# Optimization experiments

Measured on AMD Instinct MI355X. Metric: run time of the kernel, lower is better.

The kernel has to match this reference:

```python
import jax, jax.numpy as jnp
import numpy as np

INF = 1e10
EPS = 1e-5
B, S, H, NH = 4, 1024, 1024, 16


def _linear(x, W, b):
    return x @ W + b


def _layernorm(x, g, b):
    mean = x.mean(-1, keepdims=True)
    var = ((x - mean) ** 2).mean(-1, keepdims=True)  # biased, matches .pow(2).mean
    return g * (x - mean) / jnp.sqrt(var + EPS) + b


def _mha(xq, xkv, mask, Wq, bq, Wk, bk, Wv, bv, Wo, bo, num_head):
    Bq, Sq, Hd = xq.shape
    d = Hd // num_head
    scale = jnp.asarray(np.sqrt(d), xq.dtype)
    q = _linear(xq, Wq, bq).reshape(Bq, Sq, num_head, d).transpose(0, 2, 1, 3)
    k = _linear(xkv, Wk, bk).reshape(Bq, -1, num_head, d).transpose(0, 2, 1, 3)
    v = _linear(xkv, Wv, bv).reshape(Bq, -1, num_head, d).transpose(0, 2, 1, 3)
    scores = jnp.einsum('bhqd,bhkd->bhqk', q, k) / scale
    # mask [B,Skv] -> additive; NOTE: original divides (scores+mask) by scale AGAIN
    add = (1.0 - mask[:, None, None, :].astype(scores.dtype)) * (-INF)
    att = jax.nn.softmax((scores + add) / scale, axis=-1)
    out = jnp.einsum('bhqk,bhkd->bhqd', att, v).transpose(0, 2, 1, 3).reshape(Bq, Sq, Hd)
    return _linear(out, Wo, bo)


def _block(hidden_states, self_att_mask, cross_hidden_states, cross_att_mask,
           sWq, sbq, sWk, sbk, sWv, sbv, sWo, sbo,
           cWq, cbq, cWk, cbk, cWv, cbv, cWo, cbo,
           g, b, W1, b1, W2, b2, num_head):
    sa = _mha(hidden_states, hidden_states, self_att_mask,
              sWq, sbq, sWk, sbk, sWv, sbv, sWo, sbo, num_head)
    sa_n = _layernorm(sa + hidden_states, g, b)
    ca = _mha(sa_n, cross_hidden_states, cross_att_mask,
              cWq, cbq, cWk, cbk, cWv, cbv, cWo, cbo, num_head)
    # NOTE: residual uses the ORIGINAL hidden_states, matching the source
    h = _layernorm(ca + hidden_states, g, b)
    ff = _linear(jax.nn.relu(_linear(h, W1, b1)), W2, b2)
    return _layernorm(ff + h, g, b)


def setup_inputs() -> dict:
    key = jax.random.key(0)
    ks = jax.random.split(key, 20)
    std = 0.02
    def lin(k, din, dout):
        k1, k2 = jax.random.split(k)
        return (jax.random.normal(k1, (din, dout), jnp.float32) * std,
                jax.random.normal(k2, (dout,), jnp.float32) * std)
    inp = {
        'hidden_states': jax.random.normal(ks[0], (B, S, H), jnp.float32),
        'self_att_mask': jnp.ones((B, S), jnp.int32),
        'cross_hidden_states': jax.random.normal(ks[1], (B, S, H), jnp.float32),
        'cross_att_mask': jnp.ones((B, S), jnp.int32),
        'num_head': NH,
    }
    names = ['sWq sbq', 'sWk sbk', 'sWv sbv', 'sWo sbo',
             'cWq cbq', 'cWk cbk', 'cWv cbv', 'cWo cbo']
    for i, nm in enumerate(names):
        wn, bn = nm.split()
        W, bb = lin(ks[2 + i], H, H)
        inp[wn] = W
        inp[bn] = bb
    inp['g'] = jnp.ones((H,), jnp.float32)
    inp['b'] = jnp.zeros((H,), jnp.float32)
    inp['W1'], inp['b1'] = lin(ks[12], H, 4 * H)
    inp['W2'], inp['b2'] = lin(ks[13], 4 * H, H)
    return inp


def reference(hidden_states, self_att_mask, cross_hidden_states, cross_att_mask,
              num_head, sWq, sbq, sWk, sbk, sWv, sbv, sWo, sbo,
              cWq, cbq, cWk, cbk, cWv, cbv, cWo, cbo,
              g, b, W1, b1, W2, b2):
    return _block(hidden_states, self_att_mask, cross_hidden_states, cross_att_mask,
                  sWq, sbq, sWk, sbk, sWv, sbv, sWo, sbo,
                  cWq, cbq, cWk, cbk, cWv, cbv, cWo, cbo,
                  g, b, W1, b1, W2, b2, num_head)
```

## Files before the change

### kernel.cpp

```cpp
#include <hip/hip_runtime.h>
#include <hip/hip_bf16.h>


typedef float float4v __attribute__((ext_vector_type(4)));
typedef __bf16 bf16x8 __attribute__((ext_vector_type(8)));
typedef unsigned short ushort8 __attribute__((ext_vector_type(8)));
typedef unsigned int uint2v __attribute__((ext_vector_type(2)));

#define VBIG (1 << 29)

__device__ __forceinline__ unsigned short f2bf1(float f) {
    unsigned u = __builtin_bit_cast(unsigned, f);
    u += 0x7fffu + ((u >> 16) & 1u);
    return (unsigned short)(u >> 16);
}
__device__ __forceinline__ unsigned f2bf2(float lo, float hi) {
    unsigned a = __builtin_bit_cast(unsigned, lo);
    a += 0x7fffu + ((a >> 16) & 1u);
    unsigned b = __builtin_bit_cast(unsigned, hi);
    b += 0x7fffu + ((b >> 16) & 1u);
    return (a >> 16) | (b & 0xffff0000u);
}
__device__ __forceinline__ float4v bf4_to_f4(uint2v u) {
    float4v r;
    r.x = __builtin_bit_cast(float, (u.x & 0xffffu) << 16);
    r.y = __builtin_bit_cast(float, u.x & 0xffff0000u);
    r.z = __builtin_bit_cast(float, (u.y & 0xffffu) << 16);
    r.w = __builtin_bit_cast(float, u.y & 0xffff0000u);
    return r;
}
__device__ __forceinline__ bf16x8 ldsv8(const unsigned short* p) {
    return __builtin_bit_cast(bf16x8, *(const ushort8*)p);
}
__device__ __forceinline__ void async16(const unsigned short* g, unsigned short* l) {
    __builtin_amdgcn_global_load_lds(
        (const __attribute__((address_space(1))) unsigned int*)(g),
        (__attribute__((address_space(3))) unsigned int*)(l),
        16, 0, 0);
}

template <int RELU, int DBUF>
__device__ __forceinline__ void gemm_core(
    const unsigned short* __restrict__ A, const unsigned short* __restrict__ Bt,
    const float* __restrict__ bias, unsigned short* __restrict__ Cout,
    int m0, int n0, int K, int KL, int kbase, int ldc,
    float qs, int vrel, unsigned short* __restrict__ VTout, size_t outoff)
{
    __shared__ __align__(16) unsigned short As[(DBUF ? 2 : 1) * 128 * 64];
    __shared__ __align__(16) unsigned short Bs[(DBUF ? 2 : 1) * 128 * 64];

    const int tid = threadIdx.x;
    const int w = tid >> 6, lane = tid & 63;
    const int lr = lane & 15, quad = lane >> 4;
    const int wm = (w >> 1) * 64, wn = (w & 1) * 64;

    const int sr = lane >> 3, sc = lane & 7;
    const int fch = sc ^ sr;
    const unsigned short* Ag = A + (size_t)(m0 + w * 32 + sr) * K + kbase + fch * 8;
    const unsigned short* Bg = Bt + (size_t)(n0 + w * 32 + sr) * K + kbase + fch * 8;

    float4v acc[4][4];
#pragma unroll
    for (int i = 0; i < 4; i++)
#pragma unroll
        for (int j = 0; j < 4; j++) acc[i][j] = 0.f;

    const int ch0 = quad ^ (lr & 7);
    const int ch1 = (4 + quad) ^ (lr & 7);

    auto issue = [&](int buf, int k0) {
        unsigned short* Al = &As[buf * (128 * 64) + (w * 32) * 64];
        unsigned short* Bl = &Bs[buf * (128 * 64) + (w * 32) * 64];
#pragma unroll
        for (int i = 0; i < 4; i++) {
            async16(Ag + (size_t)(i * 8) * K + k0, Al + (i * 8) * 64);
            async16(Bg + (size_t)(i * 8) * K + k0, Bl + (i * 8) * 64);
        }
    };
    auto compute = [&](int buf) {
        const unsigned short* Ab = &As[buf * (128 * 64)];
        const unsigned short* Bb = &Bs[buf * (128 * 64)];
#pragma unroll
        for (int kk = 0; kk < 2; kk++) {
            const int ch = kk ? ch1 : ch0;
            bf16x8 af[4], bf[4];
#pragma unroll
            for (int i = 0; i < 4; i++) {
                af[i] = ldsv8(&Ab[(wm + i * 16 + lr) * 64 + ch * 8]);
                bf[i] = ldsv8(&Bb[(wn + i * 16 + lr) * 64 + ch * 8]);
            }
#pragma unroll
            for (int i = 0; i < 4; i++)
#pragma unroll
                for (int j = 0; j < 4; j++)
                    acc[i][j] = __builtin_amdgcn_mfma_f32_16x16x32_bf16(af[i], bf[j], acc[i][j], 0, 0, 0);
        }
    };

    if (DBUF) {
        const int NIT = KL >> 6;
        issue(0, 0);
        for (int it = 0; it < NIT; ++it) {
            const int nxt = it + 1;
            if (nxt < NIT) {
                issue(nxt & 1, nxt << 6);
                __builtin_amdgcn_sched_barrier(0);
                __builtin_amdgcn_s_waitcnt(0x0F78);
            } else {
                __builtin_amdgcn_sched_barrier(0);
                __builtin_amdgcn_s_waitcnt(0x0F70);
            }
            __builtin_amdgcn_s_barrier();
            __builtin_amdgcn_sched_barrier(0);
            compute(it & 1);
            __builtin_amdgcn_sched_barrier(0);
            __builtin_amdgcn_s_barrier();
            __builtin_amdgcn_sched_barrier(0);
        }
    } else {
        for (int k0 = 0; k0 < KL; k0 += 64) {
            issue(0, k0);
            __syncthreads();
            compute(0);
            __syncthreads();
        }
    }

    if (vrel >= 0) {
        const int crel = vrel + wn;
        const int hh = crel >> 6;
        const int bidx = (m0 + wm) >> 10;
        const int tbase = ((m0 + wm) & 1023) + quad * 16;
#pragma unroll
        for (int j = 0; j < 4; j++) {
            const float bv = bias ? bias[n0 + wn + j * 16 + lr] : 0.f;
            const int d = j * 16 + lr;
            unsigned short* vp = VTout + ((size_t)(bidx * 16 + hh) * 64 + d) * 1024 + tbase;
#pragma unroll
            for (int r = 0; r < 4; r++) {
                uint2v u = { f2bf2(acc[0][j][r] + bv, acc[1][j][r] + bv),
                             f2bf2(acc[2][j][r] + bv, acc[3][j][r] + bv) };
                *(uint2v*)(vp + r * 4) = u;
            }
        }
        return;
    }

#pragma unroll
    for (int j = 0; j < 4; j++) {
        const int col = n0 + wn + j * 16 + lr;
        const float bv = bias ? bias[col] : 0.f;
#pragma unroll
        for (int i = 0; i < 4; i++) {
            const int row0 = m0 + wm + i * 16 + quad * 4;
#pragma unroll
            for (int r = 0; r < 4; r++) {
                float v = (acc[i][j][r] + bv) * qs;
                if (RELU) v = fmaxf(v, 0.f);
                Cout[outoff + (size_t)(row0 + r) * ldc + col] = f2bf1(v);
            }
        }
    }
}

template <int RELU, int DBUF>
__global__ __launch_bounds__(256) void gemm_bt(
    const unsigned short* __restrict__ A, const unsigned short* __restrict__ Bt,
    const float* __restrict__ bias, unsigned short* __restrict__ Cout,
    int M, int N, int K, int ldc, int order, int qcols, int vcol0,
    unsigned short* __restrict__ VTout)
{
    const int m0 = (order ? blockIdx.x : blockIdx.y) * 128;
    const int n0 = (order ? blockIdx.y : blockIdx.x) * 128;
    const int KL = K / gridDim.z;
    const int kbase = blockIdx.z * KL;
    const float qs = (n0 < qcols) ? 0.015625f : 1.0f;
    const int vrel = (n0 >= vcol0) ? n0 - vcol0 : -1;
    const size_t outoff = (size_t)blockIdx.z * M * ldc;
    gemm_core<RELU, DBUF>(A, Bt, bias, Cout, m0, n0, K, KL, kbase, ldc,
                          qs, vrel, VTout, outoff);
}

__global__ __launch_bounds__(256) void gemm_cross(
    const unsigned short* __restrict__ SANb, const unsigned short* __restrict__ WtCWQ,
    const float* __restrict__ cbq, unsigned short* __restrict__ CQ,
    const unsigned short* __restrict__ cxb, const unsigned short* __restrict__ WtCKV,
    const float* __restrict__ biasC, unsigned short* __restrict__ CKb,
    unsigned short* __restrict__ VTc)
{
    const int m0 = blockIdx.x * 128;
    const int y = blockIdx.y;
    const unsigned short *Ax, *Btx;
    const float* bx;
    unsigned short* Cx = nullptr;
    unsigned short* vt = nullptr;
    int n0, ldc = 1024, vrel = -1;
    float qs = 1.0f;
    if (y < 8) {
        Ax = SANb; Btx = WtCWQ; bx = cbq; Cx = CQ; n0 = y * 128; qs = 0.015625f;
    } else {
        Ax = cxb; Btx = WtCKV; bx = biasC; n0 = (y - 8) * 128;
        if (n0 < 1024) Cx = CKb;
        else { vrel = n0 - 1024; vt = VTc; }
    }
    gemm_core<0, 0>(Ax, Btx, bx, Cx, m0, n0, 1024, 1024, 0, ldc, qs, vrel, vt, 0);
}

__global__ __launch_bounds__(256) void attn_mfma(
    const unsigned short* __restrict__ Q, int qs,
    const unsigned short* __restrict__ K, int kvs,
    const unsigned short* __restrict__ VT,
    const float* __restrict__ maskf,
    unsigned short* __restrict__ O)
{
    __shared__ __align__(16) unsigned short Ks[2][64 * 64];
    __shared__ __align__(16) unsigned short Vt[2][64 * 64];
    __shared__ __align__(16) unsigned short Pb[64 * 64];
    __shared__ float msk[1024];

    const int bid = blockIdx.x;
    const int jdx = (bid & 7) * 128 + (bid >> 3);
    const int q0 = (jdx & 15) * 64, h = (jdx >> 4) & 15, b = jdx >> 8;
    const int tid = threadIdx.x;
    const int w = tid >> 6, lane = tid & 63;
    const int lr = lane & 15, quad = lane >> 4;
    const int wm = w * 16;
    const float4v zf = {0.f, 0.f, 0.f, 0.f};

    ((float4v*)msk)[tid] = ((const float4v*)(maskf + b * 1024))[tid];

    bf16x8 qf[2];
#pragma unroll
    for (int c = 0; c < 2; c++)
        qf[c] = ldsv8(Q + (size_t)(b * 1024 + q0 + wm + lr) * qs
                      + h * 64 + c * 32 + quad * 8);

    const int sr = lane >> 3, sc = lane & 7;
    const int fch = sc ^ sr;
    const int ch0 = quad ^ (lr & 7), ch1 = (4 + quad) ^ (lr & 7);
    const unsigned short* VTb = VT + (size_t)(b * 16 + h) * 64 * 1024;

    __syncthreads();

    float4v oac[4];
    float lsum[4];
#pragma unroll
    for (int jj = 0; jj < 4; jj++) { oac[jj] = zf; lsum[jj] = 0.f; }

    auto issue = [&](int kb, int buf) {
        const int s0 = kb * 64;
#pragma unroll
        for (int i = 0; i < 2; i++) {
            async16(K + (size_t)(b * 1024 + s0 + w * 16 + i * 8 + sr) * kvs + h * 64 + fch * 8,
                    &Ks[buf][(w * 16 + i * 8) * 64]);
            async16(VTb + (size_t)(w * 16 + i * 8 + sr) * 1024 + s0 + fch * 8,
                    &Vt[buf][(w * 16 + i * 8) * 64]);
        }
    };

    issue(0, 0);
    for (int kb = 0; kb < 16; ++kb) {
        const int cur = kb & 1;
        const int nxt = kb + 1;
        if (nxt < 16) {
            issue(nxt, nxt & 1);
            __builtin_amdgcn_sched_barrier(0);
            __builtin_amdgcn_s_waitcnt(0x0F74);
        } else {
            __builtin_amdgcn_sched_barrier(0);
            __builtin_amdgcn_s_waitcnt(0x0F70);
        }
        __builtin_amdgcn_s_barrier();
        __builtin_amdgcn_sched_barrier(0);

        float mf[4];
#pragma unroll
        for (int jj = 0; jj < 4; jj++)
            mf[jj] = msk[kb * 64 + jj * 16 + lr];

        float4v sa[4];
        __builtin_amdgcn_s_setprio(1);
#pragma unroll
        for (int jj = 0; jj < 4; jj++) {
            const int krow = jj * 16 + lr;
            bf16x8 kf0 = ldsv8(&Ks[cur][krow * 64 + ch0 * 8]);
            bf16x8 kf1 = ldsv8(&Ks[cur][krow * 64 + ch1 * 8]);
            sa[jj] = __builtin_amdgcn_mfma_f32_16x16x32_bf16(qf[0], kf0, zf, 0, 0, 0);
            sa[jj] = __builtin_amdgcn_mfma_f32_16x16x32_bf16(qf[1], kf1, sa[jj], 0, 0, 0);
        }
        __builtin_amdgcn_s_setprio(0);

#pragma unroll
        for (int rr = 0; rr < 4; rr++) {
            const float p0 = __expf(sa[0][rr]) * mf[0];
            const float p1 = __expf(sa[1][rr]) * mf[1];
            const float p2 = __expf(sa[2][rr]) * mf[2];
            const float p3 = __expf(sa[3][rr]) * mf[3];
            lsum[rr] += (p0 + p1) + (p2 + p3);
            const int row = wm + quad * 4 + rr;
            const int schp = (lr >> 1) ^ (row & 7);
            uint2v pk = { f2bf2(p0, p1), f2bf2(p2, p3) };
            *(uint2v*)&Pb[row * 64 + schp * 8 + (lr & 1) * 4] = pk;
        }

        bf16x8 pf[2];
#pragma unroll
        for (int c = 0; c < 2; c++)
            pf[c] = ldsv8(&Pb[(wm + lr) * 64 + (c ? ch1 : ch0) * 8]);
        __builtin_amdgcn_s_setprio(1);
#pragma unroll
        for (int jj = 0; jj < 4; jj++) {
            bf16x8 vf0 = ldsv8(&Vt[cur][(jj * 16 + lr) * 64 + ch0 * 8]);
            bf16x8 vf1 = ldsv8(&Vt[cur][(jj * 16 + lr) * 64 + ch1 * 8]);
            oac[jj] = __builtin_amdgcn_mfma_f32_16x16x32_bf16(pf[0], vf0, oac[jj], 0, 0, 0);
            oac[jj] = __builtin_amdgcn_mfma_f32_16x16x32_bf16(pf[1], vf1, oac[jj], 0, 0, 0);
        }
        __builtin_amdgcn_s_setprio(0);

        __builtin_amdgcn_sched_barrier(0);
        __builtin_amdgcn_s_barrier();
        __builtin_amdgcn_sched_barrier(0);
    }

#pragma unroll
    for (int rr = 0; rr < 4; rr++) {
        float l = lsum[rr];
        l += __shfl_xor(l, 1);
        l += __shfl_xor(l, 2);
        l += __shfl_xor(l, 4);
        l += __shfl_xor(l, 8);
        const float inv = 1.0f / l;
        const int row = q0 + wm + quad * 4 + rr;
        unsigned short* op = O + (size_t)(b * 1024 + row) * 1024 + h * 64;
#pragma unroll
        for (int jj = 0; jj < 4; jj++)
            op[jj * 16 + lr] = f2bf1(oac[jj][rr] * inv);
    }
}

#define PSTRIDE ((size_t)4096 * 1024)
__global__ __launch_bounds__(256) void add_ln_kernel(
    const unsigned short* __restrict__ P, int nparts, const float* __restrict__ lbias,
    const float* __restrict__ R,
    const float* __restrict__ g, const float* __restrict__ bb,
    float* __restrict__ outF, unsigned short* __restrict__ outB)
{
    const int row = blockIdx.x, tid = threadIdx.x;
    float4v z = ((const float4v*)(R + (size_t)row * 1024))[tid];
    for (int p = 0; p < nparts; ++p)
        z += bf4_to_f4(*(const uint2v*)(P + p * PSTRIDE + (size_t)row * 1024 + tid * 4));
    if (lbias) z += ((const float4v*)lbias)[tid];
    float s = z.x + z.y + z.z + z.w;
    float sq = z.x * z.x + z.y * z.y + z.z * z.z + z.w * z.w;
#pragma unroll
    for (int off = 32; off > 0; off >>= 1) {
        s += __shfl_down(s, off);
        sq += __shfl_down(sq, off);
    }
    __shared__ float ws[4], wsq[4];
    __shared__ float sm, sr;
    if ((tid & 63) == 0) { ws[tid >> 6] = s; wsq[tid >> 6] = sq; }
    __syncthreads();
    if (tid == 0) {
        float S1 = ws[0] + ws[1] + ws[2] + ws[3];
        float S2 = wsq[0] + wsq[1] + wsq[2] + wsq[3];
        float mean = S1 * (1.0f / 1024.0f);
        float var = S2 * (1.0f / 1024.0f) - mean * mean;
        sm = mean;
        sr = rsqrtf(var + 1e-5f);
    }
    __syncthreads();
    const float mean = sm, rstd = sr;
    const float4v* g4 = (const float4v*)g;
    const float4v* b4 = (const float4v*)bb;
    float4v res = g4[tid] * ((z - mean) * rstd) + b4[tid];
    if (outF) ((float4v*)(outF + (size_t)row * 1024))[tid] = res;
    if (outB) {
        uint2v u = { f2bf2(res.x, res.y), f2bf2(res.z, res.w) };
        *(uint2v*)(outB + (size_t)row * 1024 + tid * 4) = u;
    }
}

__device__ __forceinline__ void tconv_body(const float* __restrict__ S,
                                           unsigned short* __restrict__ D,
                                           int R, int C, int r0, int c0)
{
    __shared__ float tile[64][65];
    const int tid = threadIdx.x;
    const int tr = tid >> 4, tc4 = (tid & 15) * 4;
#pragma unroll
    for (int i = 0; i < 4; i++) {
        const int rr = i * 16 + tr;
        *(float4v*)&tile[rr][tc4] = *(const float4v*)(S + (size_t)(r0 + rr) * C + c0 + tc4);
    }
    __syncthreads();
#pragma unroll
    for (int i = 0; i < 4; i++) {
        const int dr = i * 16 + tr;
        float v0 = tile[tc4 + 0][dr];
        float v1 = tile[tc4 + 1][dr];
        float v2 = tile[tc4 + 2][dr];
        float v3 = tile[tc4 + 3][dr];
        uint2v u = { f2bf2(v0, v1), f2bf2(v2, v3) };
        *(uint2v*)(D + (size_t)(c0 + dr) * R + r0 + tc4) = u;
    }
}

__global__ __launch_bounds__(256) void prep_all(
    const float* __restrict__ x, const float* __restrict__ cx,
    unsigned short* __restrict__ xb, unsigned short* __restrict__ cxb,
    const float* s0, const float* s1, const float* s2, const float* s3,
    const float* s4, const float* s5, const float* s6, const float* s7,
    unsigned short* d0, unsigned short* d1, unsigned short* d2, unsigned short* d3,
    unsigned short* d4, unsigned short* d5, unsigned short* d6, unsigned short* d7,
    const float* __restrict__ W1, unsigned short* __restrict__ WtW1,
    const float* __restrict__ W2, unsigned short* __restrict__ WtW2,
    const float* __restrict__ sbq, const float* __restrict__ sbk, const float* __restrict__ sbv,
    const float* __restrict__ cbk, const float* __restrict__ cbv,
    const int* __restrict__ smask, const int* __restrict__ cmask,
    float* __restrict__ bq, float* __restrict__ bc,
    float* __restrict__ smf, float* __restrict__ cmf)
{
    const int bid = blockIdx.x, tid = threadIdx.x;
    if (bid < 8192) {
        const float* s = bid < 4096 ? x : cx;
        unsigned short* d = bid < 4096 ? xb : cxb;
        const size_t i = ((size_t)(bid & 4095) * 256 + tid) * 4;
        float4v v = *(const float4v*)(s + i);
        uint2v u = { f2bf2(v.x, v.y), f2bf2(v.z, v.w) };
        *(uint2v*)(d + i) = u;
    } else if (bid < 10240) {
        const int t = bid - 8192;
        const int which = t >> 8, sub = t & 255;
        const float* S;
        unsigned short* D;
        switch (which) {
            case 0: S = s0; D = d0; break;
            case 1: S = s1; D = d1; break;
            case 2: S = s2; D = d2; break;
            case 3: S = s3; D = d3; break;
            case 4: S = s4; D = d4; break;
            case 5: S = s5; D = d5; break;
            case 6: S = s6; D = d6; break;
            default: S = s7; D = d7; break;
        }
        tconv_body(S, D, 1024, 1024, (sub >> 4) * 64, (sub & 15) * 64);
    } else if (bid < 11264) {
        const int t = bid - 10240;
        tconv_body(W1, WtW1, 1024, 4096, (t >> 6) * 64, (t & 63) * 64);
    } else if (bid < 12288) {
        const int t = bid - 11264;
        tconv_body(W2, WtW2, 4096, 1024, (t & 63) * 64, (t >> 6) * 64);
    } else {
        const int i = (bid - 12288) * 256 + tid;
        if (i < 3072)
            bq[i] = i < 1024 ? sbq[i] : (i < 2048 ? sbk[i - 1024] : sbv[i - 2048]);
        else if (i < 5120) {
            const int j = i - 3072;
            bc[j] = j < 1024 ? cbk[j] : cbv[j - 1024];
        } else if (i < 9216)
            smf[i - 5120] = (float)smask[i - 5120];
        else
            cmf[i - 9216] = (float)cmask[i - 9216];
    }
}

extern "C" void kernel_launch(void* const* d_in, const int* in_sizes, int n_in,
                              void* d_out, int out_size, void* d_ws, size_t ws_size,
                              hipStream_t stream)
{
    const float* x     = (const float*)d_in[0];
    const int*   smask = (const int*)d_in[1];
    const float* cx    = (const float*)d_in[2];
    const int*   cmask = (const int*)d_in[3];
    const float* sWq = (const float*)d_in[5],  *sbq = (const float*)d_in[6];
    const float* sWk = (const float*)d_in[7],  *sbk = (const float*)d_in[8];
    const float* sWv = (const float*)d_in[9],  *sbv = (const float*)d_in[10];
    const float* sWo = (const float*)d_in[11], *sbo = (const float*)d_in[12];
    const float* cWq = (const float*)d_in[13], *cbq = (const float*)d_in[14];
    const float* cWk = (const float*)d_in[15], *cbk = (const float*)d_in[16];
    const float* cWv = (const float*)d_in[17], *cbv = (const float*)d_in[18];
    const float* cWo = (const float*)d_in[19], *cbo = (const float*)d_in[20];
    const float* g   = (const float*)d_in[21], *bb  = (const float*)d_in[22];
    const float* W1  = (const float*)d_in[23], *b1  = (const float*)d_in[24];
    const float* W2  = (const float*)d_in[25], *b2  = (const float*)d_in[26];
    float* out = (float*)d_out;

    const size_t MB = 1024 * 1024;
    unsigned char* ws = (unsigned char*)d_ws;
    unsigned short* xb   = (unsigned short*)(ws + 0 * MB);
    unsigned short* cxb  = (unsigned short*)(ws + 8 * MB);
    unsigned short* SANb = (unsigned short*)(ws + 16 * MB);
    unsigned short* CQ   = (unsigned short*)(ws + 24 * MB);
    unsigned short* MID  = (unsigned short*)(ws + 0 * MB);
    unsigned short* QK   = (unsigned short*)(ws + 32 * MB);
    unsigned short* VTs  = (unsigned short*)(ws + 48 * MB);
    unsigned short* P    = (unsigned short*)(ws + 32 * MB);
    unsigned short* CKb  = (unsigned short*)(ws + 56 * MB);
    unsigned short* VTc  = (unsigned short*)(ws + 64 * MB);
    unsigned short* T    = (unsigned short*)(ws + 72 * MB);
    float*          HH   = (float*)(ws + 80 * MB);
    unsigned short* HHb  = (unsigned short*)(ws + 96 * MB);
    unsigned short* WtQKV = (unsigned short*)(ws + 104 * MB);
    unsigned short* WtCKV = (unsigned short*)(ws + 110 * MB);
    unsigned short* WtSWO = (unsigned short*)(ws + 114 * MB);
    unsigned short* WtCWQ = (unsigned short*)(ws + 116 * MB);
    unsigned short* WtCWO = (unsigned short*)(ws + 118 * MB);
    unsigned short* WtW1  = (unsigned short*)(ws + 120 * MB);
    unsigned short* WtW2  = (unsigned short*)(ws + 128 * MB);
    float* biasQ = (float*)(ws + 136 * MB);
    float* biasC = (float*)(ws + 136 * MB + 16 * 1024);
    float* smf   = (float*)(ws + 136 * MB + 32 * 1024);
    float* cmf   = (float*)(ws + 136 * MB + 48 * 1024);

    dim3 blk(256);

    prep_all<<<12340, blk, 0, stream>>>(
        x, cx, xb, cxb,
        sWq, sWk, sWv, cWk, cWv, sWo, cWq, cWo,
        WtQKV, WtQKV + 1024 * 1024, WtQKV + 2 * 1024 * 1024,
        WtCKV, WtCKV + 1024 * 1024,
        WtSWO, WtCWQ, WtCWO,
        W1, WtW1, W2, WtW2,
        sbq, sbk, sbv, cbk, cbv, smask, cmask, biasQ, biasC, smf, cmf);

    gemm_bt<0, 0><<<dim3(32, 24), blk, 0, stream>>>(
        xb, WtQKV, biasQ, QK, 4096, 3072, 1024, 2048, 1, 1024, 2048, VTs);
    attn_mfma<<<1024, blk, 0, stream>>>(QK, 2048, QK + 1024, 2048, VTs, smf, T);
    gemm_bt<0, 1><<<dim3(32, 8, 2), blk, 0, stream>>>(
        T, WtSWO, nullptr, P, 4096, 1024, 1024, 1024, 1, 0, VBIG, nullptr);
    add_ln_kernel<<<4096, blk, 0, stream>>>(P, 2, sbo, x, g, bb, nullptr, SANb);

    gemm_cross<<<dim3(32, 24), blk, 0, stream>>>(
        SANb, WtCWQ, cbq, CQ, cxb, WtCKV, biasC, CKb, VTc);
    attn_mfma<<<1024, blk, 0, stream>>>(CQ, 1024, CKb, 1024, VTc, cmf, T);
    gemm_bt<0, 1><<<dim3(32, 8, 2), blk, 0, stream>>>(
        T, WtCWO, nullptr, P, 4096, 1024, 1024, 1024, 1, 0, VBIG, nullptr);
    add_ln_kernel<<<4096, blk, 0, stream>>>(P, 2, cbo, x, g, bb, HH, HHb);

    gemm_bt<1, 0><<<dim3(32, 32), blk, 0, stream>>>(
        HHb, WtW1, b1, MID, 4096, 4096, 1024, 4096, 0, 0, VBIG, nullptr);
    gemm_bt<0, 1><<<dim3(32, 8, 2), blk, 0, stream>>>(
        MID, WtW2, nullptr, P, 4096, 1024, 4096, 1024, 1, 0, VBIG, nullptr);
    add_ln_kernel<<<4096, blk, 0, stream>>>(P, 2, b2, HH, g, bb, out, nullptr);
}
```

Measured before the change: 486.4 us.

## Double-buffer GEMM with 32-wide K tiles and raise split-K to four

Replaces the single-buffered 64-wide K-tile GEMM path with a double-buffered pipeline over 32-wide K tiles that uses a new swizzle, so global-to-LDS loads overlap MFMA compute in the QKV and W1 GEMMs. The output-projection and W2 GEMMs move from split-K 2 to split-K 4 on this new path, and the LayerNorm kernels now reduce four partials. The aim is to hide load latency and add parallelism in the N=1024 GEMMs. The cost is more partial-sum traffic to P and a reduction step per LayerNorm, plus more barriers per unit of K.

```diff
diff --git a/kernel.cpp b/kernel.cpp
--- a/kernel.cpp
+++ b/kernel.cpp
@@ -39,65 +39,115 @@
         16, 0, 0);
 }
 
-template <int RELU, int DBUF>
+template <int RELU, int MODE>
 __device__ __forceinline__ void gemm_core(
     const unsigned short* __restrict__ A, const unsigned short* __restrict__ Bt,
     const float* __restrict__ bias, unsigned short* __restrict__ Cout,
     int m0, int n0, int K, int KL, int kbase, int ldc,
     float qs, int vrel, unsigned short* __restrict__ VTout, size_t outoff)
 {
-    __shared__ __align__(16) unsigned short As[(DBUF ? 2 : 1) * 128 * 64];
-    __shared__ __align__(16) unsigned short Bs[(DBUF ? 2 : 1) * 128 * 64];
+    constexpr int BUFSZ = MODE ? 8192 : 4096;
+    __shared__ __align__(16) unsigned short As[2][BUFSZ];
+    __shared__ __align__(16) unsigned short Bs[2][BUFSZ];
 
     const int tid = threadIdx.x;
     const int w = tid >> 6, lane = tid & 63;
     const int lr = lane & 15, quad = lane >> 4;
     const int wm = (w >> 1) * 64, wn = (w & 1) * 64;
 
-    const int sr = lane >> 3, sc = lane & 7;
-    const int fch = sc ^ sr;
-    const unsigned short* Ag = A + (size_t)(m0 + w * 32 + sr) * K + kbase + fch * 8;
-    const unsigned short* Bg = Bt + (size_t)(n0 + w * 32 + sr) * K + kbase + fch * 8;
-
     float4v acc[4][4];
 #pragma unroll
     for (int i = 0; i < 4; i++)
 #pragma unroll
         for (int j = 0; j < 4; j++) acc[i][j] = 0.f;
 
-    const int ch0 = quad ^ (lr & 7);
-    const int ch1 = (4 + quad) ^ (lr & 7);
-
-    auto issue = [&](int buf, int k0) {
-        unsigned short* Al = &As[buf * (128 * 64) + (w * 32) * 64];
-        unsigned short* Bl = &Bs[buf * (128 * 64) + (w * 32) * 64];
-#pragma unroll
-        for (int i = 0; i < 4; i++) {
-            async16(Ag + (size_t)(i * 8) * K + k0, Al + (i * 8) * 64);
-            async16(Bg + (size_t)(i * 8) * K + k0, Bl + (i * 8) * 64);
-        }
-    };
-    auto compute = [&](int buf) {
-        const unsigned short* Ab = &As[buf * (128 * 64)];
-        const unsigned short* Bb = &Bs[buf * (128 * 64)];
-#pragma unroll
-        for (int kk = 0; kk < 2; kk++) {
-            const int ch = kk ? ch1 : ch0;
+    if constexpr (MODE == 0) {
+        const int sr = lane >> 2, sc = lane & 3;
+        const int gch = (sc ^ ((lane >> 3) & 3)) * 8;
+        const unsigned short* Ag = A + (size_t)(m0 + w * 16 + sr) * K + kbase + gch;
+        const unsigned short* Bg = Bt + (size_t)(n0 + w * 16 + sr) * K + kbase + gch;
+        const int ch2 = (quad ^ ((lr >> 1) & 3)) * 8;
+
+        auto issue32 = [&](int buf, int k0) {
+            unsigned short* Al = &As[buf][(w * 16) * 32];
+            unsigned short* Bl = &Bs[buf][(w * 16) * 32];
+            async16(Ag + k0, Al);
+            async16(Ag + (size_t)64 * K + k0, Al + 64 * 32);
+            async16(Bg + k0, Bl);
+            async16(Bg + (size_t)64 * K + k0, Bl + 64 * 32);
+        };
+        auto compute32 = [&](int buf) {
+            const unsigned short* Ab = As[buf];
+            const unsigned short* Bb = Bs[buf];
             bf16x8 af[4], bf[4];
 #pragma unroll
             for (int i = 0; i < 4; i++) {
-                af[i] = ldsv8(&Ab[(wm + i * 16 + lr) * 64 + ch * 8]);
-                bf[i] = ldsv8(&Bb[(wn + i * 16 + lr) * 64 + ch * 8]);
+                af[i] = ldsv8(&Ab[(wm + i * 16 + lr) * 32 + ch2]);
+                bf[i] = ldsv8(&Bb[(wn + i * 16 + lr) * 32 + ch2]);
             }
 #pragma unroll
             for (int i = 0; i < 4; i++)
 #pragma unroll
                 for (int j = 0; j < 4; j++)
                     acc[i][j] = __builtin_amdgcn_mfma_f32_16x16x32_bf16(af[i], bf[j], acc[i][j], 0, 0, 0);
-        }
-    };
-
-    if (DBUF) {
+        };
+
+        const int NIT = KL >> 5;
+        issue32(0, 0);
+        for (int it = 0; it < NIT; ++it) {
+            const int nxt = it + 1;
+            if (nxt < NIT) {
+                issue32(nxt & 1, nxt << 5);
+                __builtin_amdgcn_sched_barrier(0);
+                __builtin_amdgcn_s_waitcnt(0x0F74);
+            } else {
+                __builtin_amdgcn_sched_barrier(0);
+                __builtin_amdgcn_s_waitcnt(0x0F70);
+            }
+            __builtin_amdgcn_s_barrier();
+            __builtin_amdgcn_sched_barrier(0);
+            compute32(it & 1);
+            __builtin_amdgcn_sched_barrier(0);
+            __builtin_amdgcn_s_barrier();
+            __builtin_amdgcn_sched_barrier(0);
+        }
+    } else {
+        const int sr = lane >> 3, sc = lane & 7;
+        const int fch = sc ^ sr;
+        const unsigned short* Ag = A + (size_t)(m0 + w * 32 + sr) * K + kbase + fch * 8;
+        const unsigned short* Bg = Bt + (size_t)(n0 + w * 32 + sr) * K + kbase + fch * 8;
+        const int ch0 = quad ^ (lr & 7);
+        const int ch1 = (4 + quad) ^ (lr & 7);
+
+        auto issue = [&](int buf, int k0) {
+            unsigned short* Al = &As[buf][(w * 32) * 64];
+            unsigned short* Bl = &Bs[buf][(w * 32) * 64];
+#pragma unroll
+            for (int i = 0; i < 4; i++) {
+                async16(Ag + (size_t)(i * 8) * K + k0, Al + (i * 8) * 64);
+                async16(Bg + (size_t)(i * 8) * K + k0, Bl + (i * 8) * 64);
+            }
+        };
+        auto compute = [&](int buf) {
+            const unsigned short* Ab = As[buf];
+            const unsigned short* Bb = Bs[buf];
+#pragma unroll
+            for (int kk = 0; kk < 2; kk++) {
+                const int ch = kk ? ch1 : ch0;
+                bf16x8 af[4], bf[4];
+#pragma unroll
+                for (int i = 0; i < 4; i++) {
+                    af[i] = ldsv8(&Ab[(wm + i * 16 + lr) * 64 + ch * 8]);
+                    bf[i] = ldsv8(&Bb[(wn + i * 16 + lr) * 64 + ch * 8]);
+                }
+#pragma unroll
+                for (int i = 0; i < 4; i++)
+#pragma unroll
+                    for (int j = 0; j < 4; j++)
+                        acc[i][j] = __builtin_amdgcn_mfma_f32_16x16x32_bf16(af[i], bf[j], acc[i][j], 0, 0, 0);
+            }
+        };
+
         const int NIT = KL >> 6;
         issue(0, 0);
         for (int it = 0; it < NIT; ++it) {
@@ -117,13 +167,6 @@
             __builtin_amdgcn_s_barrier();
             __builtin_amdgcn_sched_barrier(0);
         }
-    } else {
-        for (int k0 = 0; k0 < KL; k0 += 64) {
-            issue(0, k0);
-            __syncthreads();
-            compute(0);
-            __syncthreads();
-        }
     }
 
     if (vrel >= 0) {
@@ -163,7 +206,7 @@
     }
 }
 
-template <int RELU, int DBUF>
+template <int RELU, int MODE>
 __global__ __launch_bounds__(256) void gemm_bt(
     const unsigned short* __restrict__ A, const unsigned short* __restrict__ Bt,
     const float* __restrict__ bias, unsigned short* __restrict__ Cout,
@@ -177,7 +220,7 @@
     const float qs = (n0 < qcols) ? 0.015625f : 1.0f;
     const int vrel = (n0 >= vcol0) ? n0 - vcol0 : -1;
     const size_t outoff = (size_t)blockIdx.z * M * ldc;
-    gemm_core<RELU, DBUF>(A, Bt, bias, Cout, m0, n0, K, KL, kbase, ldc,
+    gemm_core<RELU, MODE>(A, Bt, bias, Cout, m0, n0, K, KL, kbase, ldc,
                           qs, vrel, VTout, outoff);
 }
 
@@ -527,20 +570,20 @@
     gemm_bt<0, 0><<<dim3(32, 24), blk, 0, stream>>>(
         xb, WtQKV, biasQ, QK, 4096, 3072, 1024, 2048, 1, 1024, 2048, VTs);
     attn_mfma<<<1024, blk, 0, stream>>>(QK, 2048, QK + 1024, 2048, VTs, smf, T);
-    gemm_bt<0, 1><<<dim3(32, 8, 2), blk, 0, stream>>>(
+    gemm_bt<0, 0><<<dim3(32, 8, 4), blk, 0, stream>>>(
         T, WtSWO, nullptr, P, 4096, 1024, 1024, 1024, 1, 0, VBIG, nullptr);
-    add_ln_kernel<<<4096, blk, 0, stream>>>(P, 2, sbo, x, g, bb, nullptr, SANb);
+    add_ln_kernel<<<4096, blk, 0, stream>>>(P, 4, sbo, x, g, bb, nullptr, SANb);
 
     gemm_cross<<<dim3(32, 24), blk, 0, stream>>>(
         SANb, WtCWQ, cbq, CQ, cxb, WtCKV, biasC, CKb, VTc);
     attn_mfma<<<1024, blk, 0, stream>>>(CQ, 1024, CKb, 1024, VTc, cmf, T);
-    gemm_bt<0, 1><<<dim3(32, 8, 2), blk, 0, stream>>>(
+    gemm_bt<0, 0><<<dim3(32, 8, 4), blk, 0, stream>>>(
         T, WtCWO, nullptr, P, 4096, 1024, 1024, 1024, 1, 0, VBIG, nullptr);
-    add_ln_kernel<<<4096, blk, 0, stream>>>(P, 2, cbo, x, g, bb, HH, HHb);
+    add_ln_kernel<<<4096, blk, 0, stream>>>(P, 4, cbo, x, g, bb, HH, HHb);
 
     gemm_bt<1, 0><<<dim3(32, 32), blk, 0, stream>>>(
         HHb, WtW1, b1, MID, 4096, 4096, 1024, 4096, 0, 0, VBIG, nullptr);
-    gemm_bt<0, 1><<<dim3(32, 8, 2), blk, 0, stream>>>(
+    gemm_bt<0, 0><<<dim3(32, 8, 4), blk, 0, stream>>>(
         MID, WtW2, nullptr, P, 4096, 1024, 4096, 1024, 1, 0, VBIG, nullptr);
-    add_ln_kernel<<<4096, blk, 0, stream>>>(P, 2, b2, HH, g, bb, out, nullptr);
-}
+    add_ln_kernel<<<4096, blk, 0, stream>>>(P, 4, b2, HH, g, bb, out, nullptr);
+}
```

Result: slower. 533.1 us (+9.6%).
